# Optimization experiments

Hardware: AMD Instinct MI355X
Metric: run time of the kernel (lower is better)

## Reference

```python
import jax, jax.numpy as jnp
import numpy as np

H = 400   # hidden_size
K = 10    # attention mixture components
V = 77    # window/vocab size
O = 121   # output_size


def lstm_layer(x_seq, W_ih, W_hh, b, h0, c0):
    """Full-sequence LSTM (PyTorch gate order i,f,g,o). x_seq: (B,T,D) -> (B,T,H)."""
    pre = jnp.einsum('btd,gd->btg', x_seq, W_ih) + b  # precompute input contribution
    W_hh_T = W_hh.T

    def step(carry, p_t):
        h, c = carry
        g = p_t + h @ W_hh_T
        i, f, gg, o = jnp.split(g, 4, axis=-1)
        c = jax.nn.sigmoid(f) * c + jax.nn.sigmoid(i) * jnp.tanh(gg)
        h = jax.nn.sigmoid(o) * jnp.tanh(c)
        return (h, c), h

    _, hs = jax.lax.scan(step, (h0, c0), pre.transpose(1, 0, 2))
    return hs.transpose(1, 0, 2)


def setup_inputs():
    key = jax.random.key(0)
    ks = jax.random.split(key, 12)
    B, T, U = 64, 600, 64
    d1, d23 = 3 + V, 3 + V + H
    s = 0.05  # ~sqrt(1/H), matching torch LSTM init scale
    p = lambda k, sh, sc=s: jax.random.normal(k, sh, jnp.float32) * sc
    return dict(
        inputs=jax.random.normal(ks[0], (B, T, 3), jnp.float32),
        text=jax.random.randint(ks[1], (B, U), 0, V),
        text_mask=jnp.ones((B, U), jnp.float32),
        W_ih1=p(ks[2], (4 * H, d1)), W_hh1=p(ks[3], (4 * H, H)), b1=jnp.zeros((4 * H,), jnp.float32),
        W_ih2=p(ks[4], (4 * H, d23)), W_hh2=p(ks[5], (4 * H, H)), b2=jnp.zeros((4 * H,), jnp.float32),
        W_ih3=p(ks[6], (4 * H, d23)), W_hh3=p(ks[7], (4 * H, H)), b3=jnp.zeros((4 * H,), jnp.float32),
        W_win=p(ks[8], (3 * K, H), 0.01), b_win=jnp.zeros((3 * K,), jnp.float32),
        W_out=p(ks[9], (O, 3 * H), 0.1), b_out=jnp.zeros((O,), jnp.float32),
    )


def reference(inputs, text, text_mask, W_ih1, W_hh1, b1, W_ih2, W_hh2, b2,
              W_ih3, W_hh3, b3, W_win, b_win, W_out, b_out):
    B, T, _ = inputs.shape
    U = text.shape[1]
    enc = jax.nn.one_hot(text, V, dtype=inputs.dtype)        # (B,U,V)
    u = jnp.arange(U, dtype=inputs.dtype)                    # char positions
    W_ih1_T, W_hh1_T = W_ih1.T, W_hh1.T

    def step1(carry, x_t):
        h, c, w, kap = carry
        inp = jnp.concatenate([x_t, w], axis=-1)             # (B, 3+V)
        g = inp @ W_ih1_T + h @ W_hh1_T + b1
        i, f, gg, o = jnp.split(g, 4, axis=-1)
        c = jax.nn.sigmoid(f) * c + jax.nn.sigmoid(i) * jnp.tanh(gg)
        h = jax.nn.sigmoid(o) * jnp.tanh(c)
        # Gaussian-mixture attention window
        mix = jnp.exp(h @ W_win.T + b_win)                   # (B, 3K)
        alpha, beta, kappa = jnp.split(mix, 3, axis=-1)      # each (B,K)
        kap = kap + kappa
        phi = jnp.sum(alpha[:, :, None] * jnp.exp(-beta[:, :, None] * (kap[:, :, None] - u) ** 2), axis=1)  # (B,U)
        phi = phi * text_mask
        w = jnp.einsum('bu,buv->bv', phi, enc)               # (B,V)
        return (h, c, w, kap), (h, w)

    zH = jnp.zeros((B, H), inputs.dtype)
    init = (zH, zH, jnp.zeros((B, V), inputs.dtype), jnp.zeros((B, K), inputs.dtype))
    _, (h1s, ws) = jax.lax.scan(step1, init, inputs.transpose(1, 0, 2))
    hid1 = h1s.transpose(1, 0, 2)                            # (B,T,H)
    wvec = ws.transpose(1, 0, 2)                             # (B,T,V)

    hid2 = lstm_layer(jnp.concatenate([inputs, hid1, wvec], axis=-1), W_ih2, W_hh2, b2, zH, zH)
    hid3 = lstm_layer(jnp.concatenate([inputs, hid2, wvec], axis=-1), W_ih3, W_hh3, b3, zH, zH)
    y_hat = jnp.concatenate([hid1, hid2, hid3], axis=-1) @ W_out.T + b_out  # (B,T,O)
    return y_hat
```

## Files before the change

kernel.cpp:

```cpp
#include <hip/hip_runtime.h>
#include <hip/hip_cooperative_groups.h>

namespace cg = cooperative_groups;

#define HH 400
#define NK 10
#define VV 77
#define NO 121
#define TT 600
#define UU 64

#define NWG 256
#define NTH 1024

#define KS  5
#define J1  12
#define J23 22
#define JO  30

#define O_L1  0
#define O_L2  384000
#define O_L3  1088000
#define O_OUT 1792000
#define O_WW  1868800
#define O_XC  1874800

typedef _Float16 h2 __attribute__((ext_vector_type(2)));

struct Args {
  const float* __restrict__ x;
  const int*   __restrict__ text;
  const float* __restrict__ mask;
  const float* __restrict__ Wih1; const float* __restrict__ Whh1; const float* __restrict__ b1;
  const float* __restrict__ Wih2; const float* __restrict__ Whh2; const float* __restrict__ b2;
  const float* __restrict__ Wih3; const float* __restrict__ Whh3; const float* __restrict__ b3;
  const float* __restrict__ Wwin; const float* __restrict__ bwin;
  const float* __restrict__ Wout; const float* __restrict__ bout;
  float* __restrict__ out;
  float* __restrict__ ws;
};

__device__ __forceinline__ float sigm(float v) { return 1.0f / (1.0f + __expf(-v)); }

#if defined(__has_builtin)
#if __has_builtin(__builtin_amdgcn_fdot2)
#define FDOT2(a,b,c) __builtin_amdgcn_fdot2((a),(b),(c),false)
#endif
#endif
#ifndef FDOT2
#define FDOT2(a,b,c) fmaf((float)(a).x,(float)(b).x, fmaf((float)(a).y,(float)(b).y,(c)))
#endif

__device__ __forceinline__ h2 toh2(unsigned int u) { return __builtin_bit_cast(h2, u); }

__device__ __forceinline__ float dot4(uint4 p, uint4 v, float a) {
  a = FDOT2(toh2(p.x), toh2(v.x), a);
  a = FDOT2(toh2(p.y), toh2(v.y), a);
  a = FDOT2(toh2(p.z), toh2(v.z), a);
  a = FDOT2(toh2(p.w), toh2(v.w), a);
  return a;
}

__device__ __forceinline__ unsigned int packh2(float f0, float f1) {
  unsigned short lo = __builtin_bit_cast(unsigned short, (_Float16)f0);
  unsigned short hi = __builtin_bit_cast(unsigned short, (_Float16)f1);
  return (unsigned int)lo | ((unsigned int)hi << 16);
}

__global__ __launch_bounds__(1024) void hsnet_kernel(Args A) {
  cg::grid_group grid = cg::this_grid();
  const int lid  = threadIdx.x;
  const int bid  = blockIdx.x;
  const int band = bid & 7;
  const int grp  = bid >> 3;
  const int lane = lid & 63;
  const int wv   = lid >> 6;
  unsigned int* __restrict__ wsu = (unsigned int*)A.ws;

  for (int i = bid * NTH + lid; i < O_XC; i += NWG * NTH) {
    float f0, f1;
    if (i < O_OUT) {
      const float *Wih, *Whh; int J, LD, rel;
      if (i < O_L2)      { rel = i;          J = J1;  LD = 80;  Wih = A.Wih1; Whh = A.Whh1; }
      else if (i < O_L3) { rel = i - O_L2;   J = J23; LD = 480; Wih = A.Wih2; Whh = A.Whh2; }
      else               { rel = i - O_L3;   J = J23; LD = 480; Wih = A.Wih3; Whh = A.Whh3; }
      int U = rel >> 2, c4 = rel & 3;
      int r = U % 200, T = U / 200;
      int j = T % J,  T2 = T / J;
      int s = T2 % KS, b = T2 / KS;
      int cell = b * 50 + (r % 50), gate = r / 50;
      int grow = gate * 400 + cell;
      int kk = (s * J + j) * 8 + 2 * c4;
      if (kk < LD) { f0 = Wih[grow * LD + kk];        f1 = Wih[grow * LD + kk + 1]; }
      else         { f0 = Whh[grow * 400 + kk - LD];  f1 = Whh[grow * 400 + kk - LD + 1]; }
    } else if (i < O_WW) {
      int rel = i - O_OUT;
      int U = rel >> 2, c4 = rel & 3;
      int o16 = U % 16, T = U / 16;
      int j = T % JO, T2 = T / JO;
      int s = T2 % KS, b = T2 / KS;
      int oglob = 8 * o16 + b;
      int kk = (s * JO + j) * 8 + 2 * c4;
      f0 = (oglob < NO) ? A.Wout[oglob * 1200 + kk]     : 0.f;
      f1 = (oglob < NO) ? A.Wout[oglob * 1200 + kk + 1] : 0.f;
    } else {
      int u = i - O_WW, ln = u / 100, p = u - ln * 100;
      int gw = ln >> 1, half = ln & 1, k0 = half * 200 + 2 * p;
      f0 = A.Wwin[gw * HH + k0]; f1 = A.Wwin[gw * HH + k0 + 1];
    }
    wsu[i] = packh2(f0, f1);
  }
  {
    unsigned long long* xz = (unsigned long long*)(wsu + O_XC);
    for (int i = bid * NTH + lid; i < 32 * 1200; i += NWG * NTH)
      __hip_atomic_store(&xz[i], 0ull, __ATOMIC_RELAXED, __HIP_MEMORY_SCOPE_AGENT);
  }
  grid.sync();

  const uint4* W1b = (const uint4*)(wsu + O_L1)  + (size_t)band * KS * J1  * 200;
  const uint4* W2b = (const uint4*)(wsu + O_L2)  + (size_t)band * KS * J23 * 200;
  const uint4* W3b = (const uint4*)(wsu + O_L3)  + (size_t)band * KS * J23 * 200;
  const uint4* WOb = (const uint4*)(wsu + O_OUT) + (size_t)band * KS * JO  * 16;
  const unsigned int* __restrict__ WWIN = wsu + O_WW;
  unsigned long long* xg = (unsigned long long*)(wsu + O_XC) + (size_t)grp * 1200;

  __shared__ alignas(16) _Float16 svh1[2][480];
  __shared__ alignas(16) _Float16 svh2[2][880];
  __shared__ alignas(16) _Float16 svh3[2][880];
  __shared__ alignas(16) _Float16 soh[2][1200];
  __shared__ float pp[2000];
  __shared__ float pO[160];

  for (int i = lid; i < 960;  i += NTH) (&svh1[0][0])[i] = (_Float16)0.f;
  for (int i = lid; i < 1760; i += NTH) { (&svh2[0][0])[i] = (_Float16)0.f;
                                          (&svh3[0][0])[i] = (_Float16)0.f; }
  for (int i = lid; i < 2400; i += NTH) (&soh[0][0])[i] = (_Float16)0.f;
  if (lid >= 512 && lid < 518) {
    int il = (lid - 512) / 3, cm = (lid - 512) % 3;
    svh1[il][cm] = (_Float16)A.x[(size_t)(2 * grp + il) * TT * 3 + cm];
  }

  const int rg = lid % 200;
  const int sg = lid / 200;
  const int itm = 2 * grp + ((wv < 2) ? wv : 0);
  float maskr = A.mask[itm * UU + lane];
  int   textr = A.text[itm * UU + lane];
  float bwinr = (lane < 60 && !(lane & 1)) ? A.bwin[lane >> 1] : 0.f;
  float kapr[NK];
  #pragma unroll
  for (int k = 0; k < NK; ++k) kapr[k] = 0.f;
  float2 c1 = {0.f, 0.f}, c2r = {0.f, 0.f}, c3r = {0.f, 0.f};
  __syncthreads();

#define GATES(WB, J, V0, V1)                                                  \
    if (sg < KS) {                                                            \
      const uint4* Wp = (WB) + (size_t)(sg * (J)) * 200 + rg;                 \
      const uint4* p0 = (const uint4*)((V0) + sg * (J) * 8);                  \
      const uint4* p1 = (const uint4*)((V1) + sg * (J) * 8);                  \
      float a0 = 0.f, a1 = 0.f;                                               \
      _Pragma("unroll 2")                                                     \
      for (int j = 0; j < (J); ++j) {                                         \
        uint4 w = Wp[(size_t)j * 200];                                        \
        a0 = dot4(w, p0[j], a0); a1 = dot4(w, p1[j], a1);                     \
      }                                                                       \
      pp[(sg * 2 + 0) * 200 + rg] = a0;                                       \
      pp[(sg * 2 + 1) * 200 + rg] = a1;                                       \
    }

#define CELL(B, CREG, PH, GEN, STORES)                                        \
    if (lid < 50) {                                                           \
      int il = lid / 25, pr = lid % 25;                                       \
      float2 hp;                                                              \
      _Pragma("unroll")                                                       \
      for (int e = 0; e < 2; ++e) {                                           \
        int cl = 2 * pr + e;                                                  \
        float gI = 0.f, gF = 0.f, gG = 0.f, gO = 0.f;                         \
        _Pragma("unroll")                                                     \
        for (int s = 0; s < KS; ++s) {                                        \
          const float* b0 = &pp[(s * 2 + il) * 200];                          \
          gI += b0[cl]; gF += b0[50 + cl]; gG += b0[100 + cl]; gO += b0[150 + cl]; \
        }                                                                     \
        int gcell = band * 50 + cl;                                           \
        gI += B[gcell]; gF += B[400 + gcell]; gG += B[800 + gcell]; gO += B[1200 + gcell]; \
        float cc = sigm(gF) * (e ? CREG.y : CREG.x) + sigm(gI) * tanhf(gG);   \
        if (e) CREG.y = cc; else CREG.x = cc;                                 \
        float h = sigm(gO) * tanhf(cc);                                       \
        if (e) hp.y = h; else hp.x = h;                                       \
      }                                                                       \
      h2 hh = { (_Float16)hp.x, (_Float16)hp.y };                             \
      int idx = band * 50 + 2 * pr;                                           \
      unsigned long long tw = ((unsigned long long)(GEN) << 32)               \
                            | (unsigned long long)__builtin_bit_cast(unsigned int, hh); \
      __hip_atomic_store(&xg[(((PH) * 8 + band) * 2 + il) * 25 + pr], tw,     \
                         __ATOMIC_RELAXED, __HIP_MEMORY_SCOPE_AGENT);         \
      STORES                                                                  \
    }

#define POLL(PH, GEN, DESTS)                                                  \
    if (lid >= 64 && lid < 414) {                                             \
      int task = lid - 64;                                                    \
      int p = task / 50, w = task % 50, il = w / 25, pr = w % 25;             \
      int pb = p + (p >= band);                                               \
      const unsigned int gexp = (GEN);                                        \
      unsigned long long v64;                                                 \
      while ((unsigned int)((v64 = __hip_atomic_load(                         \
                 &xg[(((PH) * 8 + pb) * 2 + il) * 25 + pr],                   \
                 __ATOMIC_RELAXED, __HIP_MEMORY_SCOPE_AGENT)) >> 32) != gexp) \
        __builtin_amdgcn_s_sleep(1);                                          \
      h2 hv = toh2((unsigned int)v64);                                        \
      int idx = pb * 50 + 2 * pr;                                             \
      DESTS                                                                   \
    }

#define OUTS(S0, S1, LB)                                                      \
    if (lid >= (LB) && lid < (LB) + ((S1) - (S0)) * 16) {                     \
      int oi = (lid - (LB)) & 15, s = (S0) + ((lid - (LB)) >> 4);             \
      const uint4* Wp = WOb + (size_t)(s * JO) * 16 + oi;                     \
      const uint4* p0 = (const uint4*)(&soh[0][s * 240]);                     \
      const uint4* p1 = (const uint4*)(&soh[1][s * 240]);                     \
      float a0 = 0.f, a1 = 0.f;                                               \
      _Pragma("unroll 3")                                                     \
      for (int j = 0; j < JO; ++j) {                                          \
        uint4 w = Wp[(size_t)j * 16];                                         \
        a0 = dot4(w, p0[j], a0); a1 = dot4(w, p1[j], a1);                     \
      }                                                                       \
      pO[(s * 2 + 0) * 16 + oi] = a0;                                         \
      pO[(s * 2 + 1) * 16 + oi] = a1;                                         \
    }

  for (int t = 0; t < TT; ++t) {
    GATES(W1b, J1, svh1[0], svh1[1])
    __syncthreads();
    CELL(A.b1, c1, 0, 3u * t + 1u,
      soh[il][idx] = hh.x;      soh[il][idx + 1] = hh.y;
      svh1[il][80 + idx] = hh.x; svh1[il][81 + idx] = hh.y;
      svh2[il][3 + idx]  = hh.x; svh2[il][4 + idx]  = hh.y;
    )
    if (lid >= 512 && lid < 518) {
      int il = (lid - 512) / 3, cm = (lid - 512) % 3;
      _Float16 xv = (_Float16)A.x[((size_t)(2 * grp + il) * TT + t) * 3 + cm];
      svh2[il][cm] = xv; svh3[il][cm] = xv;
    }
    if (t > 0) { OUTS(3, 5, 448) }
    POLL(0, 3u * t + 1u,
      soh[il][idx] = hv.x;      soh[il][idx + 1] = hv.y;
      svh1[il][80 + idx] = hv.x; svh1[il][81 + idx] = hv.y;
      svh2[il][3 + idx]  = hv.x; svh2[il][4 + idx]  = hv.y;
    )
    __syncthreads();
    if (wv < 2) {
      const int il = wv;
      const h2* hO = (const h2*)soh[il];
      float m = 0.f;
      if (lane < 60) {
        const uint4* ww = (const uint4*)WWIN + lane * 25;
        const h2* hp = hO + (lane & 1) * 100;
        float acc = 0.f;
        #pragma unroll 5
        for (int p = 0; p < 25; ++p) {
          uint4 wq = ww[p];
          acc = FDOT2(toh2(wq.x), hp[4 * p + 0], acc);
          acc = FDOT2(toh2(wq.y), hp[4 * p + 1], acc);
          acc = FDOT2(toh2(wq.z), hp[4 * p + 2], acc);
          acc = FDOT2(toh2(wq.w), hp[4 * p + 3], acc);
        }
        m = acc;
      }
      m += __shfl_xor(m, 1);
      float mix = 0.f;
      if (lane < 60 && !(lane & 1)) mix = __expf(m + bwinr);
      float alpha[NK], beta[NK];
      #pragma unroll
      for (int k = 0; k < NK; ++k) {
        alpha[k] = __shfl(mix, 2 * k);
        beta[k]  = __shfl(mix, 20 + 2 * k);
        kapr[k] += __shfl(mix, 40 + 2 * k);
      }
      float u = (float)lane, phi = 0.f;
      #pragma unroll
      for (int k = 0; k < NK; ++k) {
        float d = kapr[k] - u;
        phi += alpha[k] * __expf(-beta[k] * d * d);
      }
      phi *= maskr;
      float w0a = 0.f, w1a = 0.f;
      #pragma unroll 8
      for (int uu2 = 0; uu2 < UU; ++uu2) {
        int   tu = __shfl(textr, uu2);
        float pu = __shfl(phi, uu2);
        w0a += (tu == lane)      ? pu : 0.f;
        w1a += (tu == lane + 64) ? pu : 0.f;
      }
      if (lane < VV) {
        _Float16 wh = (_Float16)w0a;
        svh1[il][3 + lane] = wh; svh2[il][403 + lane] = wh; svh3[il][403 + lane] = wh;
      }
      if (lane + 64 < VV) {
        _Float16 wh = (_Float16)w1a;
        svh1[il][67 + lane] = wh; svh2[il][467 + lane] = wh; svh3[il][467 + lane] = wh;
      }
    }
    if (t > 0 && lid >= 128 && lid < 160) {
      int k2 = lid - 128, oi = k2 & 15, il = k2 >> 4;
      int o = 8 * oi + band;
      if (o < NO) {
        float r = A.bout[o];
        #pragma unroll
        for (int s = 0; s < KS; ++s) r += pO[(s * 2 + il) * 16 + oi];
        A.out[((size_t)(2 * grp + il) * TT + (t - 1)) * NO + o] = r;
      }
    }
    __syncthreads();
    GATES(W2b, J23, svh2[0], svh2[1])
    __syncthreads();
    CELL(A.b2, c2r, 1, 3u * t + 2u,
      soh[il][400 + idx] = hh.x;  soh[il][401 + idx] = hh.y;
      svh2[il][480 + idx] = hh.x; svh2[il][481 + idx] = hh.y;
      svh3[il][3 + idx]   = hh.x; svh3[il][4 + idx]   = hh.y;
    )
    POLL(1, 3u * t + 2u,
      soh[il][400 + idx] = hv.x;  soh[il][401 + idx] = hv.y;
      svh2[il][480 + idx] = hv.x; svh2[il][481 + idx] = hv.y;
      svh3[il][3 + idx]   = hv.x; svh3[il][4 + idx]   = hv.y;
    )
    __syncthreads();
    GATES(W3b, J23, svh3[0], svh3[1])
    __syncthreads();
    CELL(A.b3, c3r, 2, 3u * t + 3u,
      soh[il][800 + idx] = hh.x;  soh[il][801 + idx] = hh.y;
      svh3[il][480 + idx] = hh.x; svh3[il][481 + idx] = hh.y;
    )
    if (lid >= 512 && lid < 518 && t + 1 < TT) {
      int il = (lid - 512) / 3, cm = (lid - 512) % 3;
      svh1[il][cm] = (_Float16)A.x[((size_t)(2 * grp + il) * TT + (t + 1)) * 3 + cm];
    }
    OUTS(0, 3, 448)
    POLL(2, 3u * t + 3u,
      soh[il][800 + idx] = hv.x;  soh[il][801 + idx] = hv.y;
      svh3[il][480 + idx] = hv.x; svh3[il][481 + idx] = hv.y;
    )
    __syncthreads();
  }
  OUTS(3, 5, 448)
  __syncthreads();
  if (lid < 32) {
    int oi = lid & 15, il = lid >> 4;
    int o = 8 * oi + band;
    if (o < NO) {
      float r = A.bout[o];
      #pragma unroll
      for (int s = 0; s < KS; ++s) r += pO[(s * 2 + il) * 16 + oi];
      A.out[((size_t)(2 * grp + il) * TT + (TT - 1)) * NO + o] = r;
    }
  }
#undef GATES
#undef CELL
#undef POLL
#undef OUTS
}

extern "C" void kernel_launch(void* const* d_in, const int* in_sizes, int n_in,
                              void* d_out, int out_size, void* d_ws, size_t ws_size,
                              hipStream_t stream) {
  Args a;
  a.x    = (const float*)d_in[0];
  a.text = (const int*)  d_in[1];
  a.mask = (const float*)d_in[2];
  a.Wih1 = (const float*)d_in[3];  a.Whh1 = (const float*)d_in[4];  a.b1 = (const float*)d_in[5];
  a.Wih2 = (const float*)d_in[6];  a.Whh2 = (const float*)d_in[7];  a.b2 = (const float*)d_in[8];
  a.Wih3 = (const float*)d_in[9];  a.Whh3 = (const float*)d_in[10]; a.b3 = (const float*)d_in[11];
  a.Wwin = (const float*)d_in[12]; a.bwin = (const float*)d_in[13];
  a.Wout = (const float*)d_in[14]; a.bout = (const float*)d_in[15];
  a.out  = (float*)d_out;
  a.ws   = (float*)d_ws;
  void* kargs[] = { &a };
  hipLaunchCooperativeKernel((const void*)hsnet_kernel, dim3(NWG), dim3(NTH),
                             kargs, 0, stream);
}
```

Baseline: 15.68 ms.

## Precompute layer-1 gate matvec for next step during layer-3 polling

Layer-1 gate partial sums for step t+1 are now computed by otherwise idle threads (lid>=624) during the layer-3 cell and poll phase of step t, into a new shared buffer. The layer-1 cell then reads these precomputed sums directly, which takes the layer-1 GATES pass and a barrier off the serial critical path at the start of each timestep. The x input for t+1 is loaded earlier so it is ready, and one barrier is added after initialization. The risk is that the 400 helper threads each run a 60-iteration loop alone, which may lengthen the layer-3 phase. The layer-1 inputs must also already be final when this pass runs.

```diff
diff --git a/kernel.cpp b/kernel.cpp
--- a/kernel.cpp
+++ b/kernel.cpp
@@ -129,12 +129,14 @@
   __shared__ alignas(16) _Float16 svh3[2][880];
   __shared__ alignas(16) _Float16 soh[2][1200];
   __shared__ float pp[2000];
+  __shared__ float ppL1[400];
   __shared__ float pO[160];
 
   for (int i = lid; i < 960;  i += NTH) (&svh1[0][0])[i] = (_Float16)0.f;
   for (int i = lid; i < 1760; i += NTH) { (&svh2[0][0])[i] = (_Float16)0.f;
                                           (&svh3[0][0])[i] = (_Float16)0.f; }
   for (int i = lid; i < 2400; i += NTH) (&soh[0][0])[i] = (_Float16)0.f;
+  __syncthreads();
   if (lid >= 512 && lid < 518) {
     int il = (lid - 512) / 3, cm = (lid - 512) % 3;
     svh1[il][cm] = (_Float16)A.x[(size_t)(2 * grp + il) * TT * 3 + cm];
@@ -151,6 +153,18 @@
   for (int k = 0; k < NK; ++k) kapr[k] = 0.f;
   float2 c1 = {0.f, 0.f}, c2r = {0.f, 0.f}, c3r = {0.f, 0.f};
   __syncthreads();
+
+#define L1G                                                                   \
+    if (lid >= 624) {                                                         \
+      int t4 = lid - 624, rgl = t4 % 200, ill = t4 / 200;                     \
+      const uint4* Wp = W1b + rgl;                                            \
+      const uint4* vp = (const uint4*)svh1[ill];                              \
+      float a = 0.f;                                                          \
+      _Pragma("unroll 4")                                                     \
+      for (int j = 0; j < 60; ++j)                                            \
+        a = dot4(Wp[(size_t)j * 200], vp[j], a);                              \
+      ppL1[ill * 200 + rgl] = a;                                              \
+    }
 
 #define GATES(WB, J, V0, V1)                                                  \
     if (sg < KS) {                                                            \
@@ -228,14 +242,36 @@
       pO[(s * 2 + 1) * 16 + oi] = a1;                                         \
     }
 
+  L1G
+  __syncthreads();
+
   for (int t = 0; t < TT; ++t) {
-    GATES(W1b, J1, svh1[0], svh1[1])
-    __syncthreads();
-    CELL(A.b1, c1, 0, 3u * t + 1u,
+    if (lid < 50) {
+      int il = lid / 25, pr = lid % 25;
+      float2 hp;
+      #pragma unroll
+      for (int e = 0; e < 2; ++e) {
+        int cl = 2 * pr + e;
+        int gcell = band * 50 + cl;
+        float gI = ppL1[il * 200 + cl]       + A.b1[gcell];
+        float gF = ppL1[il * 200 + 50 + cl]  + A.b1[400 + gcell];
+        float gG = ppL1[il * 200 + 100 + cl] + A.b1[800 + gcell];
+        float gO = ppL1[il * 200 + 150 + cl] + A.b1[1200 + gcell];
+        float cc = sigm(gF) * (e ? c1.y : c1.x) + sigm(gI) * tanhf(gG);
+        if (e) c1.y = cc; else c1.x = cc;
+        float h = sigm(gO) * tanhf(cc);
+        if (e) hp.y = h; else hp.x = h;
+      }
+      h2 hh = { (_Float16)hp.x, (_Float16)hp.y };
+      int idx = band * 50 + 2 * pr;
+      unsigned long long tw = ((unsigned long long)(3u * t + 1u) << 32)
+                            | (unsigned long long)__builtin_bit_cast(unsigned int, hh);
+      __hip_atomic_store(&xg[((0 * 8 + band) * 2 + il) * 25 + pr], tw,
+                         __ATOMIC_RELAXED, __HIP_MEMORY_SCOPE_AGENT);
       soh[il][idx] = hh.x;      soh[il][idx + 1] = hh.y;
       svh1[il][80 + idx] = hh.x; svh1[il][81 + idx] = hh.y;
       svh2[il][3 + idx]  = hh.x; svh2[il][4 + idx]  = hh.y;
-    )
+    }
     if (lid >= 512 && lid < 518) {
       int il = (lid - 512) / 3, cm = (lid - 512) % 3;
       _Float16 xv = (_Float16)A.x[((size_t)(2 * grp + il) * TT + t) * 3 + cm];
@@ -318,6 +354,10 @@
       svh2[il][480 + idx] = hh.x; svh2[il][481 + idx] = hh.y;
       svh3[il][3 + idx]   = hh.x; svh3[il][4 + idx]   = hh.y;
     )
+    if (lid >= 512 && lid < 518 && t + 1 < TT) {
+      int il = (lid - 512) / 3, cm = (lid - 512) % 3;
+      svh1[il][cm] = (_Float16)A.x[((size_t)(2 * grp + il) * TT + (t + 1)) * 3 + cm];
+    }
     POLL(1, 3u * t + 2u,
       soh[il][400 + idx] = hv.x;  soh[il][401 + idx] = hv.y;
       svh2[il][480 + idx] = hv.x; svh2[il][481 + idx] = hv.y;
@@ -330,11 +370,8 @@
       soh[il][800 + idx] = hh.x;  soh[il][801 + idx] = hh.y;
       svh3[il][480 + idx] = hh.x; svh3[il][481 + idx] = hh.y;
     )
-    if (lid >= 512 && lid < 518 && t + 1 < TT) {
-      int il = (lid - 512) / 3, cm = (lid - 512) % 3;
-      svh1[il][cm] = (_Float16)A.x[((size_t)(2 * grp + il) * TT + (t + 1)) * 3 + cm];
-    }
     OUTS(0, 3, 448)
+    if (t + 1 < TT) { L1G }
     POLL(2, 3u * t + 3u,
       soh[il][800 + idx] = hv.x;  soh[il][801 + idx] = hv.y;
       svh3[il][480 + idx] = hv.x; svh3[il][481 + idx] = hv.y;
@@ -353,6 +390,7 @@
       A.out[((size_t)(2 * grp + il) * TT + (TT - 1)) * NO + o] = r;
     }
   }
+#undef L1G
 #undef GATES
 #undef CELL
 #undef POLL
```

After: 16.35 ms. 4.3% more time.
